# Kernel optimization log

Hardware: AMD Instinct MI355X
Metric: run time of the kernel (lower is better)

Reference implementation:

```python
import jax, jax.numpy as jnp
import numpy as np

LEFT = 5
RIGHT = 5

def setup_inputs() -> dict:
    key = jax.random.key(0)
    k1, k2 = jax.random.split(key)
    x = jax.random.normal(k1, (32, 2000, 80), dtype=jnp.float32)
    lengths = jax.random.uniform(k2, (32,), dtype=jnp.float32)
    return {"x": x, "lengths": lengths}

def reference(x, lengths):
    # x: [B, T, C]. The torch module's grouped conv1d with a one-hot eye kernel
    # is exactly a sliding-window gather: output channel (c, i) at time t equals
    # x[t + i - LEFT, c] with zero padding outside [0, T).
    B, T, C = x.shape
    ctx_len = LEFT + RIGHT + 1
    x_pad = jnp.pad(x, ((0, 0), (LEFT, RIGHT), (0, 0)))  # [B, T+L+R, C]
    # stack shifted views: ctx[b, t, c, i] = x[t + i - LEFT, c]
    ctx = jnp.stack([x_pad[:, i:i + T, :] for i in range(ctx_len)], axis=-1)  # [B,T,C,ctx_len]
    # torch conv output channel order is channel-major (c fastest over ctx index)
    cw_x = ctx.reshape(B, T, C * ctx_len)
    # length masking: len_abs = round(T * lengths); mask[b, t] = t < len_abs[b]
    len_abs = jnp.round(T * lengths).astype(jnp.int32)
    mask = (jnp.arange(T)[None, :] < len_abs[:, None]).astype(cw_x.dtype)  # [B, T]
    return cw_x * mask[:, :, None]
```

## Files before the change

kernel.cpp:

```cpp
#include <hip/hip_runtime.h>

#define BB    32
#define TT    2000
#define CC    80
#define CTX   11
#define LEFTP 5

#define TL    20
#define NROWS (TL + 2 * LEFTP)
#define S     84
#define ROWQ  220
#define NTILE (TT / TL)

typedef float fvec4 __attribute__((ext_vector_type(4)));

__global__ __launch_bounds__(256) void context_window_kernel(
    const float* __restrict__ x,
    const float* __restrict__ lengths,
    float* __restrict__ out)
{
    __shared__ float lds[NROWS * S];

    const int tile = blockIdx.x % NTILE;
    const int b    = blockIdx.x / NTILE;
    const int t0   = tile * TL;
    const int tid  = threadIdx.x;

    const int len = __float2int_rn((float)TT * lengths[b]);

    fvec4* outq = (fvec4*)out + ((size_t)b * TT + t0) * ROWQ;

    if (t0 >= len) {
        const fvec4 z = (fvec4)0.f;
        for (int o = tid; o < TL * ROWQ; o += 256)
            __builtin_nontemporal_store(z, &outq[o]);
        return;
    }

    const fvec4* xb4 = (const fvec4*)(x + (size_t)b * TT * CC);
    for (int idx = tid; idx < NROWS * (CC / 4); idx += 256) {
        int r    = idx / (CC / 4);
        int c4   = idx - r * (CC / 4);
        int trow = t0 - LEFTP + r;
        fvec4 v = (fvec4)0.f;
        if ((unsigned)trow < (unsigned)TT) v = xb4[trow * (CC / 4) + c4];
        *(fvec4*)&lds[r * S + c4 * 4] = v;
    }
    __syncthreads();

    if (tid < ROWQ) {
        int caddr[4];
#pragma unroll
        for (int j = 0; j < 4; ++j) {
            int k = 4 * tid + j;
            int c = k / CTX;
            int i = k - c * CTX;
            caddr[j] = i * S + c;
        }
        fvec4* op = outq + tid;
#pragma unroll
        for (int t4 = 0; t4 < TL; t4 += 4) {
            fvec4 v[4];
#pragma unroll
            for (int u = 0; u < 4; ++u) {
                const float* lp = &lds[(t4 + u) * S];
                v[u].x = lp[caddr[0]];
                v[u].y = lp[caddr[1]];
                v[u].z = lp[caddr[2]];
                v[u].w = lp[caddr[3]];
            }
#pragma unroll
            for (int u = 0; u < 4; ++u) {
                fvec4 w = (t0 + t4 + u < len) ? v[u] : (fvec4)0.f;
                __builtin_nontemporal_store(w, &op[(t4 + u) * ROWQ]);
            }
        }
    }
}

extern "C" void kernel_launch(void* const* d_in, const int* in_sizes, int n_in,
                              void* d_out, int out_size, void* d_ws, size_t ws_size,
                              hipStream_t stream) {
    const float* x       = (const float*)d_in[0];
    const float* lengths = (const float*)d_in[1];
    float* out           = (float*)d_out;

    const int grid = BB * NTILE;
    context_window_kernel<<<grid, 256, 0, stream>>>(x, lengths, out);
}
```

Before: 241.4 us.

## Flatten output loop over all threads with LDS offset table, larger time tile

Doubles the time tile to 40 rows and replaces the per-thread fixed-column loop, which used only 220 of 256 threads, with a flat loop over all output quads spread across every thread. Per-quad LDS gather offsets are now looked up from a small shared table. Nontemporal stores are swapped for plain stores. The aim is full thread utilisation and less halo overhead per tile, at the cost of a per-element divide and table lookup, fewer blocks, and different cache behaviour for the writes.

```diff
diff --git a/kernel.cpp b/kernel.cpp
--- a/kernel.cpp
+++ b/kernel.cpp
@@ -6,11 +6,12 @@
 #define CTX   11
 #define LEFTP 5
 
-#define TL    20
+#define TL    40
 #define NROWS (TL + 2 * LEFTP)
 #define S     84
 #define ROWQ  220
 #define NTILE (TT / TL)
+#define QPT   (TL * ROWQ)
 
 typedef float fvec4 __attribute__((ext_vector_type(4)));
 
@@ -20,6 +21,7 @@
     float* __restrict__ out)
 {
     __shared__ float lds[NROWS * S];
+    __shared__ int   lut[ROWQ * 4];
 
     const int tile = blockIdx.x % NTILE;
     const int b    = blockIdx.x / NTILE;
@@ -32,8 +34,8 @@
 
     if (t0 >= len) {
         const fvec4 z = (fvec4)0.f;
-        for (int o = tid; o < TL * ROWQ; o += 256)
-            __builtin_nontemporal_store(z, &outq[o]);
+        for (int f = tid; f < QPT; f += 256)
+            outq[f] = z;
         return;
     }
 
@@ -46,35 +48,31 @@
         if ((unsigned)trow < (unsigned)TT) v = xb4[trow * (CC / 4) + c4];
         *(fvec4*)&lds[r * S + c4 * 4] = v;
     }
-    __syncthreads();
-
     if (tid < ROWQ) {
-        int caddr[4];
+        int o[4];
 #pragma unroll
         for (int j = 0; j < 4; ++j) {
             int k = 4 * tid + j;
             int c = k / CTX;
             int i = k - c * CTX;
-            caddr[j] = i * S + c;
+            o[j] = i * S + c;
         }
-        fvec4* op = outq + tid;
-#pragma unroll
-        for (int t4 = 0; t4 < TL; t4 += 4) {
-            fvec4 v[4];
-#pragma unroll
-            for (int u = 0; u < 4; ++u) {
-                const float* lp = &lds[(t4 + u) * S];
-                v[u].x = lp[caddr[0]];
-                v[u].y = lp[caddr[1]];
-                v[u].z = lp[caddr[2]];
-                v[u].w = lp[caddr[3]];
-            }
-#pragma unroll
-            for (int u = 0; u < 4; ++u) {
-                fvec4 w = (t0 + t4 + u < len) ? v[u] : (fvec4)0.f;
-                __builtin_nontemporal_store(w, &op[(t4 + u) * ROWQ]);
-            }
-        }
+        *(int4*)&lut[tid * 4] = make_int4(o[0], o[1], o[2], o[3]);
+    }
+    __syncthreads();
+
+    for (int f = tid; f < QPT; f += 256) {
+        unsigned t = (unsigned)f / 220u;
+        unsigned q = (unsigned)f - t * 220u;
+        int4 o = *(const int4*)&lut[q * 4];
+        const float* lp = &lds[t * S];
+        fvec4 v;
+        v.x = lp[o.x];
+        v.y = lp[o.y];
+        v.z = lp[o.z];
+        v.w = lp[o.w];
+        if ((int)(t0 + t) >= len) v = (fvec4)0.f;
+        outq[f] = v;
     }
 }
 
```

New measurement: 232.7 us. -3.6%, faster.
